# Performance work log

Measured on AMD Instinct MI355X. Metric: run time of the kernel, lower is better.

## Reference

```python
import jax, jax.numpy as jnp
import numpy as np

N_NODES = 8192
DIM = 64
K = 32
ALPHA = 3.0


def setup_inputs() -> dict:
    key = jax.random.key(0)
    ks = jax.random.split(key, 6)
    scale = 1.0 / np.sqrt(DIM)
    return {
        "x": jnp.arange(N_NODES, dtype=jnp.int64) if jax.config.jax_enable_x64 else jnp.arange(N_NODES, dtype=jnp.int32),
        "emb1": jax.random.normal(ks[0], (N_NODES, DIM), dtype=jnp.float32),
        "emb2": jax.random.normal(ks[1], (N_NODES, DIM), dtype=jnp.float32),
        "W1": jax.random.normal(ks[2], (DIM, DIM), dtype=jnp.float32) * scale,
        "b1": jax.random.normal(ks[3], (DIM,), dtype=jnp.float32) * scale,
        "W2": jax.random.normal(ks[4], (DIM, DIM), dtype=jnp.float32) * scale,
        "b2": jax.random.normal(ks[5], (DIM,), dtype=jnp.float32) * scale,
    }


def reference(x, emb1, emb2, W1, b1, W2, b2):
    # Embedding lookups: [N, D]
    m1 = emb1[x]
    m2 = emb2[x]
    # Linear + tanh with alpha gain
    M1 = jnp.tanh(ALPHA * (m1 @ W1.T + b1))
    M2 = jnp.tanh(ALPHA * (m2 @ W2.T + b2))
    # Antisymmetric score matrix [N, N]
    A = M1 @ M2.T - M2 @ M1.T
    A = jax.nn.relu(jnp.tanh(ALPHA * A))
    # Row-wise top-k sparsification. Small uniform noise breaks ties
    # (matches torch's `A + rand_like(A)*0.01` before topk).
    noise = jax.random.uniform(jax.random.key(1), A.shape, dtype=A.dtype) * 0.01
    _, idx = jax.lax.top_k(A + noise, K)  # idx: [N, K]
    rows = jnp.arange(A.shape[0])[:, None]
    mask = jnp.zeros_like(A).at[rows, idx].set(1.0)
    return A * mask
```

## Files before the change

### kernel.cpp

```cpp
#include <hip/hip_runtime.h>
#include <stdint.h>

#define NN 8192
#define DD 64

__device__ float g_M1[NN * DD];
__device__ float g_M2[NN * DD];

__device__ __forceinline__ uint32_t rotl32(uint32_t v, uint32_t s) {
  return (v << s) | (v >> (32u - s));
}

__device__ __forceinline__ uint32_t tf_bits_part(uint32_t i) {
  const uint32_t ks1 = 1u, ks2 = 0x1BD11BDBu;
  uint32_t x0 = 0u;
  uint32_t x1 = i + ks1;
#define TFR4(a,b,c,d) \
  x0 += x1; x1 = rotl32(x1,a); x1 ^= x0; \
  x0 += x1; x1 = rotl32(x1,b); x1 ^= x0; \
  x0 += x1; x1 = rotl32(x1,c); x1 ^= x0; \
  x0 += x1; x1 = rotl32(x1,d); x1 ^= x0;
  TFR4(13u,15u,26u,6u)   x0 += ks1; x1 += ks2 + 1u;
  TFR4(17u,29u,16u,24u)  x0 += ks2; x1 += 2u;
  TFR4(13u,15u,26u,6u)              x1 += ks1 + 3u;
  TFR4(17u,29u,16u,24u)  x0 += ks1; x1 += ks2 + 4u;
  TFR4(13u,15u,26u,6u)   x0 += ks2; x1 += 5u;
#undef TFR4
  return x0 ^ x1;
}

__device__ __forceinline__ float noise_at(uint32_t n) {
  uint32_t bits = tf_bits_part(n);
  float u = __fadd_rn(__uint_as_float((bits >> 9) | 0x3F800000u), -1.0f);
  return __fmul_rn(u, 0.01f);
}

__device__ __forceinline__ float tanh_fam(float x) {
  const float kClamp = 7.99881172180175781f;
  float ax = fabsf(x);
  float xc = fminf(fmaxf(x, -kClamp), kClamp);
  float s = __fmul_rn(xc, xc);
  float p = -2.76076847742355e-16f;
  p = fmaf(s, p, 2.00018790482477e-13f);
  p = fmaf(s, p, -8.60467152213735e-11f);
  p = fmaf(s, p, 5.12229709037114e-08f);
  p = fmaf(s, p, 1.48572235717979e-05f);
  p = fmaf(s, p, 6.37261928875436e-04f);
  p = fmaf(s, p, 4.89352455891786e-03f);
  p = __fmul_rn(xc, p);
  float q = 1.19825839466702e-06f;
  q = fmaf(s, q, 1.18534705686654e-04f);
  q = fmaf(s, q, 2.26843463243900e-03f);
  q = fmaf(s, q, 4.89352518554385e-03f);
  float r = p / q;
  return (ax < 0.0004f) ? x : r;
}

__global__ __launch_bounds__(256) void k1_M(
    const float* __restrict__ emb1, const float* __restrict__ emb2,
    const float* __restrict__ W1, const float* __restrict__ b1,
    const float* __restrict__ W2, const float* __restrict__ b2) {
  int g = blockIdx.x * 256 + threadIdx.x;
  int d = g & 63;
  int row = (g >> 6) & (NN - 1);
  int mat = g >> 19;
  const float* emb = mat ? emb2 : emb1;
  const float* W   = mat ? W2 : W1;
  const float* bv  = mat ? b2 : b1;
  float* outm      = mat ? g_M2 : g_M1;
  const float* mrow = emb + (size_t)row * DD;
  const float* wrow = W + d * DD;
  float p = 0.0f;
  #pragma unroll
  for (int k = 0; k < DD; ++k) p = fmaf(mrow[k], wrow[k], p);
  float t = __fmul_rn(3.0f, __fadd_rn(p, bv[d]));
  outm[row * DD + d] = tanh_fam(t);
}

__global__ __launch_bounds__(256) void k2_A(float* __restrict__ out) {
  __shared__ __align__(16) float sm[4][32][68];
  const int tid = threadIdx.x;
  int rev = 8255 - (int)blockIdx.x;
  int t = (int)((sqrtf(8.0f * (float)rev + 1.0f) - 1.0f) * 0.5f);
  while ((t + 1) * (t + 2) / 2 <= rev) ++t;
  while (t * (t + 1) / 2 > rev) --t;
  const int by = 127 - t;
  const int bx = 127 - (rev - t * (t + 1) / 2);
  const int i0 = by * 64, j0 = bx * 64;
  const int tn = tid & 15, tm = tid >> 4;
  float acc1[4][4], acc2[4][4];
  #pragma unroll
  for (int m = 0; m < 4; ++m)
    #pragma unroll
    for (int n = 0; n < 4; ++n) { acc1[m][n] = 0.0f; acc2[m][n] = 0.0f; }

  for (int ph = 0; ph < 2; ++ph) {
    const int kb = ph * 32;
    __syncthreads();
    {
      const int k = tid & 31;
      const int r0 = tid >> 5;
      #pragma unroll
      for (int it = 0; it < 8; ++it) {
        const int r = r0 * 8 + it;
        sm[0][k][r] = g_M1[(i0 + r) * DD + kb + k];
        sm[1][k][r] = g_M2[(i0 + r) * DD + kb + k];
        sm[2][k][r] = g_M1[(j0 + r) * DD + kb + k];
        sm[3][k][r] = g_M2[(j0 + r) * DD + kb + k];
      }
    }
    __syncthreads();
    #pragma unroll 8
    for (int k = 0; k < 32; ++k) {
      float a1[4], a2[4], b1v[4], b2v[4];
      *(float4*)a1  = *(const float4*)&sm[0][k][tm * 4];
      *(float4*)a2  = *(const float4*)&sm[1][k][tm * 4];
      *(float4*)b1v = *(const float4*)&sm[2][k][tn * 4];
      *(float4*)b2v = *(const float4*)&sm[3][k][tn * 4];
      #pragma unroll
      for (int m = 0; m < 4; ++m)
        #pragma unroll
        for (int n = 0; n < 4; ++n) {
          acc1[m][n] = fmaf(a1[m], b2v[n], acc1[m][n]);
          acc2[m][n] = fmaf(a2[m], b1v[n], acc2[m][n]);
        }
    }
  }
  float u[4][4];
  #pragma unroll
  for (int m = 0; m < 4; ++m) {
    float o[4];
    #pragma unroll
    for (int n = 0; n < 4; ++n) {
      float tt = __fmul_rn(3.0f, __fsub_rn(acc1[m][n], acc2[m][n]));
      u[m][n] = tanh_fam(tt);
      o[n] = fmaxf(u[m][n], 0.0f);
    }
    *(float4*)&out[(size_t)(i0 + tm * 4 + m) * NN + j0 + tn * 4] = *(float4*)o;
  }
  if (by != bx) {
    #pragma unroll
    for (int n = 0; n < 4; ++n) {
      float o[4];
      #pragma unroll
      for (int m = 0; m < 4; ++m) o[m] = fmaxf(-u[m][n], 0.0f);
      *(float4*)&out[(size_t)(j0 + tn * 4 + n) * NN + i0 + tm * 4] = *(float4*)o;
    }
  }
}

__global__ __launch_bounds__(256) void k3_topk(float* __restrict__ out) {
  __shared__ __align__(16) float arow[NN];
  __shared__ uint32_t hist[256];
  __shared__ uint32_t flags[256];
  __shared__ __align__(16) unsigned long long cand[512];
  __shared__ uint32_t bkt8[NN / 4];
  __shared__ uint32_t smisc[8];
  const int tid = threadIdx.x;
  const int row = blockIdx.x;
  const float* src = out + (size_t)row * NN;
  #pragma unroll
  for (int s = 0; s < 8; ++s) {
    int q = tid + 256 * s;
    *(float4*)&arow[q * 4] = *(const float4*)&src[q * 4];
    bkt8[q] = 0xFFFFFFFFu;
  }
  hist[tid] = 0u; flags[tid] = 0u;
  if (tid < 8) smisc[tid] = 0u;
  __syncthreads();

  uint32_t qmask = 0u;
  #pragma unroll
  for (int s = 0; s < 32; ++s) {
    int j = tid + 256 * s;
    if (arow[j] >= 0.98f) qmask |= (1u << s);
  }
  {
    uint32_t qm = qmask;
    while (qm) {
      int s = __builtin_ctz(qm); qm &= qm - 1u;
      int j = tid + 256 * s;
      float key = __fadd_rn(arow[j], noise_at((uint32_t)(row * NN + j)));
      uint32_t kb = __float_as_uint(key);
      if (kb >= 0x3F800000u) {
        uint32_t bkt = (kb - 0x3F800000u) >> 9; if (bkt > 254u) bkt = 254u;
        atomicAdd(&hist[bkt], 1u);
        ((uint8_t*)bkt8)[j] = (uint8_t)bkt;
      }
    }
  }
  __syncthreads();

  if (tid < 64) {
    int bhi = 255 - 4 * tid;
    uint32_t s0 = hist[bhi] + hist[bhi - 1] + hist[bhi - 2] + hist[bhi - 3];
    uint32_t c = s0;
    #pragma unroll
    for (int dl = 1; dl < 64; dl <<= 1) {
      uint32_t t = __shfl_up(c, dl, 64);
      if (tid >= dl) c += t;
    }
    uint32_t total = __shfl(c, 63, 64);
    unsigned long long vote = __ballot(c >= 32u);
    if (total >= 32u && vote != 0ull) {
      int L = __builtin_ctzll(vote);
      if (tid == L) {
        uint32_t above = c - s0;
        int Dd = bhi - 3;
        #pragma unroll
        for (int qq = 0; qq < 4; ++qq) {
          int b = bhi - qq;
          uint32_t h = hist[b];
          if (above + h >= 32u) { Dd = b; break; }
          above += h;
        }
        smisc[2] = (uint32_t)Dd; smisc[3] = above; smisc[4] = 1u;
      }
    }
  }
  __syncthreads();

  bool ok = (smisc[4] != 0u);
  const uint32_t Dd = smisc[2];
  const uint32_t above = smisc[3];
  if (ok) {
    #pragma unroll
    for (int s = 0; s < 8; ++s) {
      int d = tid + 256 * s;
      uint32_t w = bkt8[d];
      if (w == 0xFFFFFFFFu) continue;
      #pragma unroll
      for (int b = 0; b < 4; ++b) {
        uint32_t bk = (w >> (8 * b)) & 255u;
        if (bk == 255u) continue;
        uint32_t j = (uint32_t)(d * 4 + b);
        if (bk > Dd) {
          atomicOr(&flags[j >> 5], 1u << (j & 31));
        } else if (bk == Dd) {
          uint32_t kb = __float_as_uint(
              __fadd_rn(arow[j], noise_at((uint32_t)(row * NN + j))));
          uint32_t pos = atomicAdd(&smisc[0], 1u);
          if (pos < 512u)
            cand[pos] = ((unsigned long long)kb << 32) | (uint32_t)(~j);
        }
      }
    }
    __syncthreads();
    if (tid == 0 && smisc[0] > 512u) smisc[4] = 0u;
    __syncthreads();
    ok = (smisc[4] != 0u);
    if (ok) {
      const uint32_t cnt = smisc[0];
      const uint32_t need = 32u - above;
      for (uint32_t ci = tid; ci < cnt; ci += 256u) {
        unsigned long long me = cand[ci];
        uint32_t rank = 0;
        for (uint32_t o = 0; o < cnt; ++o) rank += (cand[o] > me) ? 1u : 0u;
        if (rank < need) {
          uint32_t j = ~(uint32_t)me;
          atomicOr(&flags[j >> 5], 1u << (j & 31));
        }
      }
    }
    __syncthreads();
    ok = (smisc[4] != 0u);
  }

  if (!ok) {
    uint32_t mykb[32];
    #pragma unroll
    for (int s = 0; s < 32; ++s) {
      int j = tid + 256 * s;
      mykb[s] = __float_as_uint(__fadd_rn(arow[j], noise_at((uint32_t)(row * NN + j))));
    }
    flags[tid] = 0u;
    __syncthreads();
    for (int it = 0; it < 32; ++it) {
      unsigned long long best = 0ull;
      #pragma unroll
      for (int s = 0; s < 32; ++s) {
        int j = tid + 256 * s;
        if (((flags[j >> 5] >> (j & 31)) & 1u) == 0u) {
          unsigned long long k64 =
              ((unsigned long long)mykb[s] << 32) | (uint32_t)(~(uint32_t)j);
          if (k64 > best) best = k64;
        }
      }
      cand[tid] = best;
      __syncthreads();
      if (tid == 0) {
        unsigned long long w = 0ull;
        for (int t2 = 0; t2 < 256; ++t2) if (cand[t2] > w) w = cand[t2];
        uint32_t j = ~(uint32_t)w;
        flags[j >> 5] |= (1u << (j & 31));
      }
      __syncthreads();
    }
  }
  __syncthreads();

  float* dst = out + (size_t)row * NN;
  #pragma unroll
  for (int s = 0; s < 8; ++s) {
    int q = tid + 256 * s;
    int j = q * 4;
    float4 v = *(const float4*)&arow[j];
    uint32_t fw = flags[j >> 5] >> (j & 31);
    v.x = (fw & 1u) ? v.x : 0.0f;
    v.y = (fw & 2u) ? v.y : 0.0f;
    v.z = (fw & 4u) ? v.z : 0.0f;
    v.w = (fw & 8u) ? v.w : 0.0f;
    *(float4*)&dst[j] = v;
  }
}

extern "C" void kernel_launch(void* const* d_in, const int* in_sizes, int n_in,
                              void* d_out, int out_size, void* d_ws, size_t ws_size,
                              hipStream_t stream) {
  (void)in_sizes; (void)n_in; (void)d_ws; (void)ws_size; (void)out_size;
  const float* emb1 = (const float*)d_in[1];
  const float* emb2 = (const float*)d_in[2];
  const float* W1   = (const float*)d_in[3];
  const float* b1   = (const float*)d_in[4];
  const float* W2   = (const float*)d_in[5];
  const float* b2   = (const float*)d_in[6];
  float* out = (float*)d_out;

  hipLaunchKernelGGL(k1_M, dim3((2 * NN * DD) / 256), dim3(256), 0, stream,
                     emb1, emb2, W1, b1, W2, b2);
  hipLaunchKernelGGL(k2_A, dim3(8256), dim3(256), 0, stream, out);
  hipLaunchKernelGGL(k3_topk, dim3(NN), dim3(256), 0, stream, out);
}
```

Before: 357.6 us.

## Replace full-row shared staging with compacted candidate list in top-k kernel

The top-k kernel no longer copies the whole 8192-float row into shared memory. It keeps the row in registers, compacts only the entries above a raised cutoff into a small packed shared list, and runs the histogram and candidate selection over that list. Output is written as a zeroed row plus scattered writes of the selected values. This cuts shared-memory footprint, which may raise occupancy, and removes full-row scans. In exchange it adds scattered global stores and a fallback path that rereads the row from global memory when the list overflows.

Result: slower. 666.9 us (+86.5%).

```diff
diff --git a/kernel.cpp b/kernel.cpp
--- a/kernel.cpp
+++ b/kernel.cpp
@@ -3,6 +3,8 @@
 
 #define NN 8192
 #define DD 64
+#define LISTCAP 4608
+#define CUT 0.9899f
 
 __device__ float g_M1[NN * DD];
 __device__ float g_M2[NN * DD];
@@ -150,43 +152,62 @@
 }
 
 __global__ __launch_bounds__(256) void k3_topk(float* __restrict__ out) {
-  __shared__ __align__(16) float arow[NN];
+  __shared__ uint32_t list[LISTCAP];
+  __shared__ uint8_t  bktb[LISTCAP];
   __shared__ uint32_t hist[256];
   __shared__ uint32_t flags[256];
   __shared__ __align__(16) unsigned long long cand[512];
-  __shared__ uint32_t bkt8[NN / 4];
   __shared__ uint32_t smisc[8];
   const int tid = threadIdx.x;
   const int row = blockIdx.x;
   const float* src = out + (size_t)row * NN;
-  #pragma unroll
-  for (int s = 0; s < 8; ++s) {
-    int q = tid + 256 * s;
-    *(float4*)&arow[q * 4] = *(const float4*)&src[q * 4];
-    bkt8[q] = 0xFFFFFFFFu;
-  }
+  float* dst = out + (size_t)row * NN;
   hist[tid] = 0u; flags[tid] = 0u;
   if (tid < 8) smisc[tid] = 0u;
   __syncthreads();
 
-  uint32_t qmask = 0u;
-  #pragma unroll
-  for (int s = 0; s < 32; ++s) {
-    int j = tid + 256 * s;
-    if (arow[j] >= 0.98f) qmask |= (1u << s);
-  }
-  {
-    uint32_t qm = qmask;
-    while (qm) {
-      int s = __builtin_ctz(qm); qm &= qm - 1u;
-      int j = tid + 256 * s;
-      float key = __fadd_rn(arow[j], noise_at((uint32_t)(row * NN + j)));
-      uint32_t kb = __float_as_uint(key);
+  float4 r[8];
+  #pragma unroll
+  for (int s = 0; s < 8; ++s)
+    r[s] = *(const float4*)&src[(tid + 256 * s) * 4];
+  int myc = 0;
+  #pragma unroll
+  for (int s = 0; s < 8; ++s)
+    myc += (r[s].x >= CUT) + (r[s].y >= CUT) + (r[s].z >= CUT) + (r[s].w >= CUT);
+  uint32_t base = atomicAdd(&smisc[0], (uint32_t)myc);
+  #pragma unroll
+  for (int s = 0; s < 8; ++s) {
+    const int q = tid + 256 * s;
+    float vals[4] = {r[s].x, r[s].y, r[s].z, r[s].w};
+    #pragma unroll
+    for (int c = 0; c < 4; ++c) {
+      if (vals[c] >= CUT) {
+        uint32_t j = (uint32_t)(q * 4 + c);
+        uint32_t aoff = 0x3F800000u - __float_as_uint(vals[c]);
+        if (base < LISTCAP) list[base] = (aoff << 13) | j;
+        ++base;
+      }
+    }
+  }
+  __syncthreads();
+
+  const uint32_t cnt = smisc[0];
+  bool ok = (cnt <= LISTCAP);
+
+  if (ok) {
+    for (uint32_t i = tid; i < cnt; i += 256u) {
+      uint32_t e = list[i];
+      uint32_t j = e & 8191u;
+      float a = __uint_as_float(0x3F800000u - (e >> 13));
+      uint32_t kb = __float_as_uint(
+          __fadd_rn(a, noise_at((uint32_t)row * 8192u + j)));
+      uint32_t bk = 255u;
       if (kb >= 0x3F800000u) {
-        uint32_t bkt = (kb - 0x3F800000u) >> 9; if (bkt > 254u) bkt = 254u;
-        atomicAdd(&hist[bkt], 1u);
-        ((uint8_t*)bkt8)[j] = (uint8_t)bkt;
-      }
+        bk = (kb - 0x3F800000u) >> 9;
+        if (bk > 254u) bk = 254u;
+        atomicAdd(&hist[bk], 1u);
+      }
+      bktb[i] = (uint8_t)bk;
     }
   }
   __syncthreads();
@@ -220,42 +241,38 @@
   }
   __syncthreads();
 
-  bool ok = (smisc[4] != 0u);
+  ok = ok && (smisc[4] != 0u);
   const uint32_t Dd = smisc[2];
   const uint32_t above = smisc[3];
+
   if (ok) {
-    #pragma unroll
-    for (int s = 0; s < 8; ++s) {
-      int d = tid + 256 * s;
-      uint32_t w = bkt8[d];
-      if (w == 0xFFFFFFFFu) continue;
-      #pragma unroll
-      for (int b = 0; b < 4; ++b) {
-        uint32_t bk = (w >> (8 * b)) & 255u;
-        if (bk == 255u) continue;
-        uint32_t j = (uint32_t)(d * 4 + b);
-        if (bk > Dd) {
-          atomicOr(&flags[j >> 5], 1u << (j & 31));
-        } else if (bk == Dd) {
-          uint32_t kb = __float_as_uint(
-              __fadd_rn(arow[j], noise_at((uint32_t)(row * NN + j))));
-          uint32_t pos = atomicAdd(&smisc[0], 1u);
-          if (pos < 512u)
-            cand[pos] = ((unsigned long long)kb << 32) | (uint32_t)(~j);
-        }
-      }
-    }
-    __syncthreads();
-    if (tid == 0 && smisc[0] > 512u) smisc[4] = 0u;
+    for (uint32_t i = tid; i < cnt; i += 256u) {
+      uint32_t bk = bktb[i];
+      if (bk == 255u || bk < Dd) continue;
+      uint32_t e = list[i];
+      uint32_t j = e & 8191u;
+      if (bk > Dd) {
+        atomicOr(&flags[j >> 5], 1u << (j & 31));
+      } else {
+        float a = __uint_as_float(0x3F800000u - (e >> 13));
+        uint32_t kb = __float_as_uint(
+            __fadd_rn(a, noise_at((uint32_t)row * 8192u + j)));
+        uint32_t pos = atomicAdd(&smisc[1], 1u);
+        if (pos < 512u)
+          cand[pos] = ((unsigned long long)kb << 32) | (uint32_t)(~j);
+      }
+    }
+    __syncthreads();
+    if (tid == 0 && smisc[1] > 512u) smisc[4] = 0u;
     __syncthreads();
     ok = (smisc[4] != 0u);
     if (ok) {
-      const uint32_t cnt = smisc[0];
+      const uint32_t bcnt = smisc[1];
       const uint32_t need = 32u - above;
-      for (uint32_t ci = tid; ci < cnt; ci += 256u) {
+      for (uint32_t ci = tid; ci < bcnt; ci += 256u) {
         unsigned long long me = cand[ci];
         uint32_t rank = 0;
-        for (uint32_t o = 0; o < cnt; ++o) rank += (cand[o] > me) ? 1u : 0u;
+        for (uint32_t o = 0; o < bcnt; ++o) rank += (cand[o] > me) ? 1u : 0u;
         if (rank < need) {
           uint32_t j = ~(uint32_t)me;
           atomicOr(&flags[j >> 5], 1u << (j & 31));
@@ -266,12 +283,27 @@
     ok = (smisc[4] != 0u);
   }
 
-  if (!ok) {
+  if (ok) {
+    float4 z = make_float4(0.0f, 0.0f, 0.0f, 0.0f);
+    #pragma unroll
+    for (int s = 0; s < 8; ++s)
+      *(float4*)&dst[(tid + 256 * s) * 4] = z;
+    __syncthreads();
+    for (uint32_t i = tid; i < cnt; i += 256u) {
+      uint32_t bk = bktb[i];
+      if (bk == 255u || bk < Dd) continue;
+      uint32_t e = list[i];
+      uint32_t j = e & 8191u;
+      if ((flags[j >> 5] >> (j & 31)) & 1u)
+        dst[j] = __uint_as_float(0x3F800000u - (e >> 13));
+    }
+  } else {
     uint32_t mykb[32];
     #pragma unroll
     for (int s = 0; s < 32; ++s) {
       int j = tid + 256 * s;
-      mykb[s] = __float_as_uint(__fadd_rn(arow[j], noise_at((uint32_t)(row * NN + j))));
+      mykb[s] = __float_as_uint(
+          __fadd_rn(src[j], noise_at((uint32_t)row * 8192u + j)));
     }
     flags[tid] = 0u;
     __syncthreads();
@@ -296,21 +328,17 @@
       }
       __syncthreads();
     }
-  }
-  __syncthreads();
-
-  float* dst = out + (size_t)row * NN;
-  #pragma unroll
-  for (int s = 0; s < 8; ++s) {
-    int q = tid + 256 * s;
-    int j = q * 4;
-    float4 v = *(const float4*)&arow[j];
-    uint32_t fw = flags[j >> 5] >> (j & 31);
-    v.x = (fw & 1u) ? v.x : 0.0f;
-    v.y = (fw & 2u) ? v.y : 0.0f;
-    v.z = (fw & 4u) ? v.z : 0.0f;
-    v.w = (fw & 8u) ? v.w : 0.0f;
-    *(float4*)&dst[j] = v;
+    #pragma unroll
+    for (int s = 0; s < 8; ++s) {
+      int j = (tid + 256 * s) * 4;
+      float4 v = *(const float4*)&src[j];
+      uint32_t fw = flags[j >> 5] >> (j & 31);
+      v.x = (fw & 1u) ? v.x : 0.0f;
+      v.y = (fw & 2u) ? v.y : 0.0f;
+      v.z = (fw & 4u) ? v.z : 0.0f;
+      v.w = (fw & 8u) ? v.w : 0.0f;
+      *(float4*)&dst[j] = v;
+    }
   }
 }
 
```

## Compact above-threshold candidates into index list before histogram top-k selection

Applied to the files above, without the earlier changes.

Replaces the per-element byte bucket map with a prefix-sum compaction of candidate indices whose value is at least a raised cutoff. Noise generation, bucketing and the later selection pass then iterate over the compact list, load-balanced across threads, instead of rescanning the full row. This adds a wave scan and an extra barrier, and falls back to the slow path if the candidate count exceeds the list capacity.

New measurement: 633.2 us. 77.1% more time.

```diff
diff --git a/kernel.cpp b/kernel.cpp
--- a/kernel.cpp
+++ b/kernel.cpp
@@ -3,6 +3,8 @@
 
 #define NN 8192
 #define DD 64
+#define CUT 0.9899f
+#define IDXCAP 4608
 
 __device__ float g_M1[NN * DD];
 __device__ float g_M2[NN * DD];
@@ -154,7 +156,9 @@
   __shared__ uint32_t hist[256];
   __shared__ uint32_t flags[256];
   __shared__ __align__(16) unsigned long long cand[512];
-  __shared__ uint32_t bkt8[NN / 4];
+  __shared__ uint16_t idx[IDXCAP];
+  __shared__ uint8_t  bktl[IDXCAP];
+  __shared__ uint32_t wsum[4];
   __shared__ uint32_t smisc[8];
   const int tid = threadIdx.x;
   const int row = blockIdx.x;
@@ -163,30 +167,53 @@
   for (int s = 0; s < 8; ++s) {
     int q = tid + 256 * s;
     *(float4*)&arow[q * 4] = *(const float4*)&src[q * 4];
-    bkt8[q] = 0xFFFFFFFFu;
   }
   hist[tid] = 0u; flags[tid] = 0u;
   if (tid < 8) smisc[tid] = 0u;
   __syncthreads();
 
-  uint32_t qmask = 0u;
+  int myc = 0;
+  #pragma unroll
+  for (int s = 0; s < 32; ++s)
+    myc += (arow[tid + 256 * s] >= CUT) ? 1 : 0;
+  const uint32_t lane = (uint32_t)(tid & 63), wv = (uint32_t)(tid >> 6);
+  uint32_t inc = (uint32_t)myc;
+  #pragma unroll
+  for (int dl = 1; dl < 64; dl <<= 1) {
+    uint32_t t = __shfl_up(inc, dl, 64);
+    if (lane >= (uint32_t)dl) inc += t;
+  }
+  if (lane == 63u) wsum[wv] = inc;
+  __syncthreads();
+  uint32_t wbase = 0;
+  for (uint32_t w = 0; w < wv; ++w) wbase += wsum[w];
+  const uint32_t cnt = wsum[0] + wsum[1] + wsum[2] + wsum[3];
+  uint32_t base = wbase + inc - (uint32_t)myc;
+
   #pragma unroll
   for (int s = 0; s < 32; ++s) {
     int j = tid + 256 * s;
-    if (arow[j] >= 0.98f) qmask |= (1u << s);
-  }
-  {
-    uint32_t qm = qmask;
-    while (qm) {
-      int s = __builtin_ctz(qm); qm &= qm - 1u;
-      int j = tid + 256 * s;
-      float key = __fadd_rn(arow[j], noise_at((uint32_t)(row * NN + j)));
-      uint32_t kb = __float_as_uint(key);
+    if (arow[j] >= CUT) {
+      if (base < IDXCAP) idx[base] = (uint16_t)j;
+      ++base;
+    }
+  }
+  __syncthreads();
+
+  bool ok = (cnt <= IDXCAP);
+
+  if (ok) {
+    for (uint32_t i = tid; i < cnt; i += 256u) {
+      uint32_t j = idx[i];
+      uint32_t kb = __float_as_uint(
+          __fadd_rn(arow[j], noise_at((uint32_t)(row * NN) + j)));
+      uint32_t bk = 255u;
       if (kb >= 0x3F800000u) {
-        uint32_t bkt = (kb - 0x3F800000u) >> 9; if (bkt > 254u) bkt = 254u;
-        atomicAdd(&hist[bkt], 1u);
-        ((uint8_t*)bkt8)[j] = (uint8_t)bkt;
-      }
+        bk = (kb - 0x3F800000u) >> 9;
+        if (bk > 254u) bk = 254u;
+        atomicAdd(&hist[bk], 1u);
+      }
+      bktl[i] = (uint8_t)bk;
     }
   }
   __syncthreads();
@@ -220,42 +247,35 @@
   }
   __syncthreads();
 
-  bool ok = (smisc[4] != 0u);
+  ok = ok && (smisc[4] != 0u);
   const uint32_t Dd = smisc[2];
   const uint32_t above = smisc[3];
   if (ok) {
-    #pragma unroll
-    for (int s = 0; s < 8; ++s) {
-      int d = tid + 256 * s;
-      uint32_t w = bkt8[d];
-      if (w == 0xFFFFFFFFu) continue;
-      #pragma unroll
-      for (int b = 0; b < 4; ++b) {
-        uint32_t bk = (w >> (8 * b)) & 255u;
-        if (bk == 255u) continue;
-        uint32_t j = (uint32_t)(d * 4 + b);
-        if (bk > Dd) {
-          atomicOr(&flags[j >> 5], 1u << (j & 31));
-        } else if (bk == Dd) {
-          uint32_t kb = __float_as_uint(
-              __fadd_rn(arow[j], noise_at((uint32_t)(row * NN + j))));
-          uint32_t pos = atomicAdd(&smisc[0], 1u);
-          if (pos < 512u)
-            cand[pos] = ((unsigned long long)kb << 32) | (uint32_t)(~j);
-        }
-      }
-    }
-    __syncthreads();
-    if (tid == 0 && smisc[0] > 512u) smisc[4] = 0u;
+    for (uint32_t i = tid; i < cnt; i += 256u) {
+      uint32_t bk = bktl[i];
+      if (bk == 255u || bk < Dd) continue;
+      uint32_t j = idx[i];
+      if (bk > Dd) {
+        atomicOr(&flags[j >> 5], 1u << (j & 31));
+      } else {
+        uint32_t kb = __float_as_uint(
+            __fadd_rn(arow[j], noise_at((uint32_t)(row * NN) + j)));
+        uint32_t pos = atomicAdd(&smisc[1], 1u);
+        if (pos < 512u)
+          cand[pos] = ((unsigned long long)kb << 32) | (uint32_t)(~j);
+      }
+    }
+    __syncthreads();
+    if (tid == 0 && smisc[1] > 512u) smisc[4] = 0u;
     __syncthreads();
     ok = (smisc[4] != 0u);
     if (ok) {
-      const uint32_t cnt = smisc[0];
+      const uint32_t bcnt = smisc[1];
       const uint32_t need = 32u - above;
-      for (uint32_t ci = tid; ci < cnt; ci += 256u) {
+      for (uint32_t ci = tid; ci < bcnt; ci += 256u) {
         unsigned long long me = cand[ci];
         uint32_t rank = 0;
-        for (uint32_t o = 0; o < cnt; ++o) rank += (cand[o] > me) ? 1u : 0u;
+        for (uint32_t o = 0; o < bcnt; ++o) rank += (cand[o] > me) ? 1u : 0u;
         if (rank < need) {
           uint32_t j = ~(uint32_t)me;
           atomicOr(&flags[j >> 5], 1u << (j & 31));
```
